# Kernel optimization log

Measured on AMD Instinct MI355X. Metric: run time of the kernel, lower is better.

Reference implementation:

```python
import jax, jax.numpy as jnp
import numpy as np

S, B, IN, H, OUT, L = 512, 64, 512, 1024, 512, 2


def setup_inputs() -> dict:
    key = jax.random.key(0)
    ks = jax.random.split(key, 16)
    s = lambda k, *shape: jax.random.normal(k, shape, dtype=jnp.float32) * 0.02
    inp = {
        "x": jax.random.normal(ks[0], (S, B, IN), dtype=jnp.float32),
        "h0": jnp.zeros((L, B, H), dtype=jnp.float32),
        # layer 0 (input -> hidden)
        "Ua0": s(ks[1], IN, H), "Uc0": s(ks[2], IN, H), "Uh0": s(ks[3], IN, H),
        "wa0": jax.random.normal(ks[4], (H,), dtype=jnp.float32) * 0.02,
        "wc0": jax.random.normal(ks[5], (H,), dtype=jnp.float32) * 0.02,
        "ba0": jnp.zeros((H,), jnp.float32), "bc0": jnp.zeros((H,), jnp.float32), "bh0": jnp.zeros((H,), jnp.float32),
        # layer 1 (hidden -> hidden)
        "Ua1": s(ks[6], H, H), "Uc1": s(ks[7], H, H), "Uh1": s(ks[8], H, H),
        "wa1": jax.random.normal(ks[9], (H,), dtype=jnp.float32) * 0.02,
        "wc1": jax.random.normal(ks[10], (H,), dtype=jnp.float32) * 0.02,
        "ba1": jnp.zeros((H,), jnp.float32), "bc1": jnp.zeros((H,), jnp.float32), "bh1": jnp.zeros((H,), jnp.float32),
        # decoder
        "Wdec": s(ks[11], H, OUT), "bdec": jnp.zeros((OUT,), jnp.float32),
    }
    return inp


def _brc_layer(x, h0, Ua, Uc, Uh, wa, wc, ba, bc, bh):
    """Bistable Recurrent Cell layer over time-major x: [S, B, in] -> ([S,B,H], [B,H])."""
    # Precompute all input-to-hidden projections as one big GEMM each.
    xa = x @ Ua + ba  # [S,B,H]
    xc = x @ Uc + bc
    xh = x @ Uh + bh

    def step(h, xs):
        xa_t, xc_t, xh_t = xs
        a = 1.0 + jnp.tanh(xa_t + wa * h)
        c = jax.nn.sigmoid(xc_t + wc * h)
        h_new = c * h + (1.0 - c) * jnp.tanh(xh_t + a * h)
        return h_new, h_new

    h_last, ys = jax.lax.scan(step, h0, (xa, xc, xh))
    return ys, h_last


def reference(x, h0, Ua0, Uc0, Uh0, wa0, wc0, ba0, bc0, bh0,
              Ua1, Uc1, Uh1, wa1, wc1, ba1, bc1, bh1, Wdec, bdec):
    y0, h0_last = _brc_layer(x, h0[0], Ua0, Uc0, Uh0, wa0, wc0, ba0, bc0, bh0)
    # dropout = 0.0 -> identity between layers
    y1, h1_last = _brc_layer(y0, h0[1], Ua1, Uc1, Uh1, wa1, wc1, ba1, bc1, bh1)
    out = y1 @ Wdec + bdec  # sequential_output=True -> decode every timestep
    hidden = jnp.stack([h0_last, h1_last])  # [L, B, H]
    return out, hidden
```

## Files before the change

kernel.cpp:

```cpp
#include <hip/hip_runtime.h>
#include <math.h>

#define S_DIM 512
#define B_DIM 64
#define IN_DIM 512
#define H_DIM 1024
#define OUT_DIM 512
#define BH (B_DIM * H_DIM)

typedef unsigned short ushort_t;
typedef unsigned int uint_t;
using f32x4 = __attribute__((ext_vector_type(4))) float;
using f16x8 = __attribute__((ext_vector_type(8))) _Float16;

#define LO_SCALE 2048.0f
#define LO_INV   (1.0f / 2048.0f)

__device__ __forceinline__ void split_f16(float v, ushort_t& hi, ushort_t& lo) {
    _Float16 h = (_Float16)v;
    float r = (v - (float)h) * LO_SCALE;
    _Float16 l = (_Float16)r;
    hi = __builtin_bit_cast(ushort_t, h);
    lo = __builtin_bit_cast(ushort_t, l);
}

__device__ __forceinline__ float frcp(float x) { return __builtin_amdgcn_rcpf(x); }
__device__ __forceinline__ float fsig(float z) { return frcp(1.f + __expf(-z)); }
__device__ __forceinline__ float ftanh(float z) { return 1.f - 2.f * frcp(1.f + __expf(2.f * z)); }

__device__ __forceinline__ void gload_lds16(const ushort_t* g, ushort_t* l) {
    __builtin_amdgcn_global_load_lds(
        (const __attribute__((address_space(1))) void*)g,
        (__attribute__((address_space(3))) void*)l, 16, 0, 0);
}

__global__ __launch_bounds__(256) void transpose_split_f16(
    const float* __restrict__ W, ushort_t* __restrict__ Whi, ushort_t* __restrict__ Wlo,
    int K, int N)
{
    __shared__ float tile[32][33];
    const int k0 = blockIdx.y * 32, n0 = blockIdx.x * 32;
    const int tx = threadIdx.x & 31, ty = threadIdx.x >> 5;
#pragma unroll
    for (int r = 0; r < 32; r += 8)
        tile[ty + r][tx] = W[(size_t)(k0 + ty + r) * N + n0 + tx];
    __syncthreads();
#pragma unroll
    for (int r = 0; r < 32; r += 8) {
        ushort_t hi, lo;
        split_f16(tile[tx][ty + r], hi, lo);
        const size_t o = (size_t)(n0 + ty + r) * K + k0 + tx;
        Whi[o] = hi;
        Wlo[o] = lo;
    }
}

__global__ __launch_bounds__(256) void convert_split_f16(
    const float* __restrict__ src, ushort_t* __restrict__ dhi, ushort_t* __restrict__ dlo,
    int n)
{
    const int i = (blockIdx.x * 256 + threadIdx.x) * 4;
    if (i < n) {
        float4 v = *(const float4*)(src + i);
        ushort4 h, l;
        split_f16(v.x, h.x, l.x); split_f16(v.y, h.y, l.y);
        split_f16(v.z, h.z, l.z); split_f16(v.w, h.w, l.w);
        *(ushort4*)(dhi + i) = h;
        *(ushort4*)(dlo + i) = l;
    }
}

__global__ __launch_bounds__(256, 2) void mfma_gemm3_split(
    const ushort_t* __restrict__ Ahi, const ushort_t* __restrict__ Alo,
    const ushort_t* __restrict__ Wh0, const ushort_t* __restrict__ Wl0,
    const ushort_t* __restrict__ Wh1, const ushort_t* __restrict__ Wl1,
    const ushort_t* __restrict__ Wh2, const ushort_t* __restrict__ Wl2,
    const float* __restrict__ b0, const float* __restrict__ b1, const float* __restrict__ b2,
    float* __restrict__ C0, float* __restrict__ C1, float* __restrict__ C2,
    int M, int N, int K)
{
    const int NB = N >> 7;
    const int inner = blockIdx.x % (3 * NB);
    const int mb = blockIdx.x / (3 * NB);
    const int nb = inner % NB;
    const int z  = inner / NB;

    const ushort_t* __restrict__ Wh = (z == 0) ? Wh0 : (z == 1) ? Wh1 : Wh2;
    const ushort_t* __restrict__ Wl = (z == 0) ? Wl0 : (z == 1) ? Wl1 : Wl2;
    const float* __restrict__ bias  = (z == 0) ? b0  : (z == 1) ? b1  : b2;
    float* __restrict__ C           = (z == 0) ? C0  : (z == 1) ? C1  : C2;

    __shared__ __align__(16) ushort_t AsH[2][128 * 32];
    __shared__ __align__(16) ushort_t AsL[2][128 * 32];
    __shared__ __align__(16) ushort_t BsH[2][128 * 32];
    __shared__ __align__(16) ushort_t BsL[2][128 * 32];

    const int tid  = threadIdx.x;
    const int lane = tid & 63;
    const int wave = tid >> 6;
    const int quad = lane >> 4;
    const int l16  = lane & 15;
    const int wm   = wave >> 1;
    const int wn   = wave & 1;

    const int row0 = mb * 128;
    const int col0 = nb * 128;

    f32x4 accP[4][4] = {};
    f32x4 accQ[4][4] = {};

    auto STAGE = [&](int buf, int k0) {
#pragma unroll
        for (int i = 0; i < 2; ++i) {
            const int c  = tid + i * 256;
            const int r  = c >> 2;
            const int kc = (c & 3) ^ ((r >> 1) & 3);
            const size_t ga = (size_t)(row0 + r) * K + k0 + kc * 8;
            const size_t gb = (size_t)(col0 + r) * K + k0 + kc * 8;
            gload_lds16(Ahi + ga, &AsH[buf][c * 8]);
            gload_lds16(Alo + ga, &AsL[buf][c * 8]);
            gload_lds16(Wh  + gb, &BsH[buf][c * 8]);
            gload_lds16(Wl  + gb, &BsL[buf][c * 8]);
        }
    };

    const int nt = K >> 5;
    STAGE(0, 0);
    int cur = 0;
    const int gq = (quad ^ ((l16 >> 1) & 3)) * 8;

    for (int t = 0; t < nt; ++t) {
        __syncthreads();
        if (t + 1 < nt) STAGE(cur ^ 1, (t + 1) << 5);

        f16x8 ah[4], al[4], bh[4], bl[4];
#pragma unroll
        for (int i = 0; i < 4; ++i) {
            const int ro = (wm * 64 + i * 16 + l16) * 32 + gq;
            ah[i] = *(const f16x8*)&AsH[cur][ro];
            al[i] = *(const f16x8*)&AsL[cur][ro];
        }
#pragma unroll
        for (int j = 0; j < 4; ++j) {
            const int ro = (wn * 64 + j * 16 + l16) * 32 + gq;
            bh[j] = *(const f16x8*)&BsH[cur][ro];
            bl[j] = *(const f16x8*)&BsL[cur][ro];
        }

#pragma unroll
        for (int i = 0; i < 4; ++i)
#pragma unroll
            for (int j = 0; j < 4; ++j) {
                accP[i][j] = __builtin_amdgcn_mfma_f32_16x16x32_f16(ah[i], bh[j], accP[i][j], 0, 0, 0);
                accQ[i][j] = __builtin_amdgcn_mfma_f32_16x16x32_f16(ah[i], bl[j], accQ[i][j], 0, 0, 0);
                accQ[i][j] = __builtin_amdgcn_mfma_f32_16x16x32_f16(al[i], bh[j], accQ[i][j], 0, 0, 0);
            }
        cur ^= 1;
    }

#pragma unroll
    for (int i = 0; i < 4; ++i) {
        const int row = row0 + wm * 64 + i * 16 + quad * 4;
#pragma unroll
        for (int j = 0; j < 4; ++j) {
            const int col = col0 + wn * 64 + j * 16 + l16;
            const float bv = bias[col];
#pragma unroll
            for (int r = 0; r < 4; ++r)
                C[(size_t)(row + r) * N + col] = accP[i][j][r] + accQ[i][j][r] * LO_INV + bv;
        }
    }
}

__global__ __launch_bounds__(256, 2) void mfma_gemm_dec(
    const ushort_t* __restrict__ A, const ushort_t* __restrict__ Wt,
    const float* __restrict__ bias, float* __restrict__ C,
    int M, int N, int K)
{
    const int NB = N >> 7;
    const int mb = blockIdx.x / NB;
    const int nb = blockIdx.x % NB;

    __shared__ __align__(16) ushort_t As[2][128 * 32];
    __shared__ __align__(16) ushort_t Bs[2][128 * 32];

    const int tid  = threadIdx.x;
    const int lane = tid & 63;
    const int wave = tid >> 6;
    const int quad = lane >> 4;
    const int l16  = lane & 15;
    const int wm   = wave >> 1;
    const int wn   = wave & 1;

    const int row0 = mb * 128;
    const int col0 = nb * 128;

    f32x4 acc[4][4] = {};

    auto STAGE = [&](int buf, int k0) {
#pragma unroll
        for (int i = 0; i < 2; ++i) {
            const int c  = tid + i * 256;
            const int r  = c >> 2;
            const int kc = (c & 3) ^ ((r >> 1) & 3);
            gload_lds16(A  + (size_t)(row0 + r) * K + k0 + kc * 8, &As[buf][c * 8]);
            gload_lds16(Wt + (size_t)(col0 + r) * K + k0 + kc * 8, &Bs[buf][c * 8]);
        }
    };

    const int nt = K >> 5;
    STAGE(0, 0);
    int cur = 0;
    const int gq = (quad ^ ((l16 >> 1) & 3)) * 8;

    for (int t = 0; t < nt; ++t) {
        __syncthreads();
        if (t + 1 < nt) STAGE(cur ^ 1, (t + 1) << 5);

        f16x8 af[4], bf[4];
#pragma unroll
        for (int i = 0; i < 4; ++i)
            af[i] = *(const f16x8*)&As[cur][(wm * 64 + i * 16 + l16) * 32 + gq];
#pragma unroll
        for (int j = 0; j < 4; ++j)
            bf[j] = *(const f16x8*)&Bs[cur][(wn * 64 + j * 16 + l16) * 32 + gq];

#pragma unroll
        for (int i = 0; i < 4; ++i)
#pragma unroll
            for (int j = 0; j < 4; ++j)
                acc[i][j] = __builtin_amdgcn_mfma_f32_16x16x32_f16(af[i], bf[j], acc[i][j], 0, 0, 0);
        cur ^= 1;
    }

#pragma unroll
    for (int i = 0; i < 4; ++i) {
        const int row = row0 + wm * 64 + i * 16 + quad * 4;
#pragma unroll
        for (int j = 0; j < 4; ++j) {
            const int col = col0 + wn * 64 + j * 16 + l16;
            const float bv = bias[col];
#pragma unroll
            for (int r = 0; r < 4; ++r)
                C[(size_t)(row + r) * N + col] = acc[i][j][r] + bv;
        }
    }
}

template <bool WRITE_LO>
__global__ __launch_bounds__(256) void brc_scan_v3(
    const float* __restrict__ xa, const float* __restrict__ xc,
    const float* __restrict__ xh, const float* __restrict__ wa,
    const float* __restrict__ wc, const float* __restrict__ h_in,
    ushort_t* __restrict__ yhi, ushort_t* __restrict__ ylo,
    float* __restrict__ h_out, int T_c)
{
    const int idx = blockIdx.x * 256 + threadIdx.x;
    const int j = idx & (H_DIM - 1);
    float h = h_in[idx];
    const float waj = wa[j], wcj = wc[j];

    float pa[8], pc[8], ph[8];
#pragma unroll
    for (int d = 0; d < 8; ++d) {
        const int dd = (d < T_c) ? d : 0;
        const size_t b = (size_t)dd * BH + idx;
        pa[d] = xa[b]; pc[d] = xc[b]; ph[d] = xh[b];
    }

#pragma unroll 8
    for (int t = 0; t < T_c; ++t) {
        const int s = t & 7;
        const float ca = pa[s], cc = pc[s], ch = ph[s];
        const int tn = t + 8;
        if (tn < T_c) {
            const size_t b = (size_t)tn * BH + idx;
            pa[s] = xa[b]; pc[s] = xc[b]; ph[s] = xh[b];
        }
        const float a = 1.f + ftanh(ca + waj * h);
        const float c = fsig(cc + wcj * h);
        h = c * h + (1.f - c) * ftanh(ch + a * h);

        ushort_t hh, hl;
        split_f16(h, hh, hl);
        const size_t ob = (size_t)t * BH + idx;
        yhi[ob] = hh;
        if (WRITE_LO) ylo[ob] = hl;
    }
    h_out[idx] = h;
}

extern "C" void kernel_launch(void* const* d_in, const int* in_sizes, int n_in,
                              void* d_out, int out_size, void* d_ws, size_t ws_size,
                              hipStream_t stream) {
    const float* x    = (const float*)d_in[0];
    const float* h0   = (const float*)d_in[1];
    const float* Ua0  = (const float*)d_in[2];
    const float* Uc0  = (const float*)d_in[3];
    const float* Uh0  = (const float*)d_in[4];
    const float* wa0  = (const float*)d_in[5];
    const float* wc0  = (const float*)d_in[6];
    const float* ba0  = (const float*)d_in[7];
    const float* bc0  = (const float*)d_in[8];
    const float* bh0  = (const float*)d_in[9];
    const float* Ua1  = (const float*)d_in[10];
    const float* Uc1  = (const float*)d_in[11];
    const float* Uh1  = (const float*)d_in[12];
    const float* wa1  = (const float*)d_in[13];
    const float* wc1  = (const float*)d_in[14];
    const float* ba1  = (const float*)d_in[15];
    const float* bc1  = (const float*)d_in[16];
    const float* bh1  = (const float*)d_in[17];
    const float* Wdec = (const float*)d_in[18];
    const float* bdec = (const float*)d_in[19];

    float* outF = (float*)d_out;
    float* out_seq  = outF;
    float* h_last0  = outF + (size_t)S_DIM * B_DIM * OUT_DIM;
    float* h_last1  = h_last0 + BH;

    char* wsb = (char*)d_ws;
    size_t off = 0;
    auto alloc = [&](size_t bytes) -> void* {
        void* p = wsb + off;
        off += (bytes + 255) & ~(size_t)255;
        return p;
    };
    const size_t szL0 = (size_t)IN_DIM * H_DIM;
    const size_t szL1 = (size_t)H_DIM * H_DIM;
    const size_t szD  = (size_t)H_DIM * OUT_DIM;
    ushort_t *Wa0h = (ushort_t*)alloc(szL0 * 2), *Wa0l = (ushort_t*)alloc(szL0 * 2);
    ushort_t *Wc0h = (ushort_t*)alloc(szL0 * 2), *Wc0l = (ushort_t*)alloc(szL0 * 2);
    ushort_t *Wh0h = (ushort_t*)alloc(szL0 * 2), *Wh0l = (ushort_t*)alloc(szL0 * 2);
    ushort_t *Wa1h = (ushort_t*)alloc(szL1 * 2), *Wa1l = (ushort_t*)alloc(szL1 * 2);
    ushort_t *Wc1h = (ushort_t*)alloc(szL1 * 2), *Wc1l = (ushort_t*)alloc(szL1 * 2);
    ushort_t *Wh1h = (ushort_t*)alloc(szL1 * 2), *Wh1l = (ushort_t*)alloc(szL1 * 2);
    ushort_t *Wdh  = (ushort_t*)alloc(szD * 2),  *Wdl  = (ushort_t*)alloc(szD * 2);

    const size_t perT = (size_t)2 * B_DIM * IN_DIM * 2 + (size_t)3 * BH * 4 + (size_t)3 * BH * 2;
    int T_c = 512;
    while (T_c > 1 && off + (size_t)T_c * perT + 4096 > ws_size) T_c >>= 1;
    const size_t chunk_elems = (size_t)T_c * BH;
    const size_t xchunk_elems = (size_t)T_c * B_DIM * IN_DIM;

    ushort_t* xhib = (ushort_t*)alloc(xchunk_elems * 2);
    ushort_t* xlob = (ushort_t*)alloc(xchunk_elems * 2);
    float* g_a = (float*)alloc(chunk_elems * 4);
    float* g_c = (float*)alloc(chunk_elems * 4);
    float* g_h = (float*)alloc(chunk_elems * 4);
    ushort_t* y0h = (ushort_t*)alloc(chunk_elems * 2);
    ushort_t* y0l = (ushort_t*)alloc(chunk_elems * 2);
    ushort_t* y1h = (ushort_t*)alloc(chunk_elems * 2);

    const int n_chunks = S_DIM / T_c;
    const int Mc = T_c * B_DIM;

    transpose_split_f16<<<dim3(H_DIM / 32, IN_DIM / 32), 256, 0, stream>>>(Ua0, Wa0h, Wa0l, IN_DIM, H_DIM);
    transpose_split_f16<<<dim3(H_DIM / 32, IN_DIM / 32), 256, 0, stream>>>(Uc0, Wc0h, Wc0l, IN_DIM, H_DIM);
    transpose_split_f16<<<dim3(H_DIM / 32, IN_DIM / 32), 256, 0, stream>>>(Uh0, Wh0h, Wh0l, IN_DIM, H_DIM);
    transpose_split_f16<<<dim3(H_DIM / 32, H_DIM / 32), 256, 0, stream>>>(Ua1, Wa1h, Wa1l, H_DIM, H_DIM);
    transpose_split_f16<<<dim3(H_DIM / 32, H_DIM / 32), 256, 0, stream>>>(Uc1, Wc1h, Wc1l, H_DIM, H_DIM);
    transpose_split_f16<<<dim3(H_DIM / 32, H_DIM / 32), 256, 0, stream>>>(Uh1, Wh1h, Wh1l, H_DIM, H_DIM);
    transpose_split_f16<<<dim3(OUT_DIM / 32, H_DIM / 32), 256, 0, stream>>>(Wdec, Wdh, Wdl, H_DIM, OUT_DIM);

    dim3 blk(256);
    const int grid_g = (H_DIM / 128) * (Mc / 128) * 3;
    const int grid_d = (OUT_DIM / 128) * (Mc / 128);
    dim3 grid_scan(BH / 256);

    for (int ci = 0; ci < n_chunks; ++ci) {
        const float* x_chunk = x + (size_t)ci * Mc * IN_DIM;
        float* out_chunk = out_seq + (size_t)ci * Mc * OUT_DIM;

        convert_split_f16<<<dim3((int)(xchunk_elems / 4 / 256)), blk, 0, stream>>>(
            x_chunk, xhib, xlob, (int)xchunk_elems);

        mfma_gemm3_split<<<dim3(grid_g), blk, 0, stream>>>(
            xhib, xlob, Wa0h, Wa0l, Wc0h, Wc0l, Wh0h, Wh0l,
            ba0, bc0, bh0, g_a, g_c, g_h, Mc, H_DIM, IN_DIM);
        brc_scan_v3<true><<<grid_scan, blk, 0, stream>>>(
            g_a, g_c, g_h, wa0, wc0, (ci == 0) ? h0 : h_last0, y0h, y0l, h_last0, T_c);

        mfma_gemm3_split<<<dim3(grid_g), blk, 0, stream>>>(
            y0h, y0l, Wa1h, Wa1l, Wc1h, Wc1l, Wh1h, Wh1l,
            ba1, bc1, bh1, g_a, g_c, g_h, Mc, H_DIM, H_DIM);
        brc_scan_v3<false><<<grid_scan, blk, 0, stream>>>(
            g_a, g_c, g_h, wa1, wc1, (ci == 0) ? (h0 + BH) : h_last1, y1h, nullptr, h_last1, T_c);

        mfma_gemm_dec<<<dim3(grid_d), blk, 0, stream>>>(
            y1h, Wdh, bdec, out_chunk, Mc, OUT_DIM, H_DIM);
    }
}
```

Baseline: 1.664 ms.

## Widen split-f16 GEMM tile to 128x256 with 512 threads and triple-buffered LDS

The three-way projection GEMM now uses 512-thread blocks, each computing a 128x256 tile with 8 waves, which halves the block count and doubles B-tile reuse. LDS staging moves from double to triple buffering with explicit vmcnt waits, so loads run two tiles ahead and only one barrier is needed per iteration. Address offsets are hoisted out of the loop, and setprio raises wave priority around the MFMA block. In exchange, shared memory rises to about 144KB, allowing one block per CU. With fewer blocks there is a risk of poorer wave occupancy and tail imbalance.

Measured after the change: 1.712 ms. +2.9%, slower.

```diff
diff --git a/kernel.cpp b/kernel.cpp
--- a/kernel.cpp
+++ b/kernel.cpp
@@ -70,7 +70,7 @@
     }
 }
 
-__global__ __launch_bounds__(256, 2) void mfma_gemm3_split(
+__global__ __launch_bounds__(512, 1) void mfma_gemm3_split(
     const ushort_t* __restrict__ Ahi, const ushort_t* __restrict__ Alo,
     const ushort_t* __restrict__ Wh0, const ushort_t* __restrict__ Wl0,
     const ushort_t* __restrict__ Wh1, const ushort_t* __restrict__ Wl1,
@@ -79,7 +79,7 @@
     float* __restrict__ C0, float* __restrict__ C1, float* __restrict__ C2,
     int M, int N, int K)
 {
-    const int NB = N >> 7;
+    const int NB = N >> 8;
     const int inner = blockIdx.x % (3 * NB);
     const int mb = blockIdx.x / (3 * NB);
     const int nb = inner % NB;
@@ -90,63 +90,83 @@
     const float* __restrict__ bias  = (z == 0) ? b0  : (z == 1) ? b1  : b2;
     float* __restrict__ C           = (z == 0) ? C0  : (z == 1) ? C1  : C2;
 
-    __shared__ __align__(16) ushort_t AsH[2][128 * 32];
-    __shared__ __align__(16) ushort_t AsL[2][128 * 32];
-    __shared__ __align__(16) ushort_t BsH[2][128 * 32];
-    __shared__ __align__(16) ushort_t BsL[2][128 * 32];
+    __shared__ __align__(16) ushort_t AsH[3][128 * 32];
+    __shared__ __align__(16) ushort_t AsL[3][128 * 32];
+    __shared__ __align__(16) ushort_t BsH[3][256 * 32];
+    __shared__ __align__(16) ushort_t BsL[3][256 * 32];
 
     const int tid  = threadIdx.x;
     const int lane = tid & 63;
     const int wave = tid >> 6;
     const int quad = lane >> 4;
     const int l16  = lane & 15;
-    const int wm   = wave >> 1;
-    const int wn   = wave & 1;
+    const int wm   = wave >> 2;
+    const int wn   = wave & 3;
 
     const int row0 = mb * 128;
-    const int col0 = nb * 128;
+    const int col0 = nb * 256;
 
     f32x4 accP[4][4] = {};
     f32x4 accQ[4][4] = {};
 
-    auto STAGE = [&](int buf, int k0) {
-#pragma unroll
-        for (int i = 0; i < 2; ++i) {
-            const int c  = tid + i * 256;
-            const int r  = c >> 2;
-            const int kc = (c & 3) ^ ((r >> 1) & 3);
-            const size_t ga = (size_t)(row0 + r) * K + k0 + kc * 8;
-            const size_t gb = (size_t)(col0 + r) * K + k0 + kc * 8;
-            gload_lds16(Ahi + ga, &AsH[buf][c * 8]);
-            gload_lds16(Alo + ga, &AsL[buf][c * 8]);
-            gload_lds16(Wh  + gb, &BsH[buf][c * 8]);
-            gload_lds16(Wl  + gb, &BsL[buf][c * 8]);
-        }
+    const int ca  = tid;
+    const int ra  = ca >> 2;
+    const int ka  = (ca & 3) ^ ((ra >> 1) & 3);
+    const size_t gaoff = (size_t)(row0 + ra) * K + ka * 8;
+
+    const int cb0 = tid,        rb0 = cb0 >> 2, kb0 = (cb0 & 3) ^ ((rb0 >> 1) & 3);
+    const int cb1 = tid + 512,  rb1 = cb1 >> 2, kb1 = (cb1 & 3) ^ ((rb1 >> 1) & 3);
+    const size_t gboff0 = (size_t)(col0 + rb0) * K + kb0 * 8;
+    const size_t gboff1 = (size_t)(col0 + rb1) * K + kb1 * 8;
+
+    auto STAGE = [&](int buf, int t) {
+        const int k0 = t << 5;
+        gload_lds16(Ahi + gaoff + k0, &AsH[buf][ca * 8]);
+        gload_lds16(Alo + gaoff + k0, &AsL[buf][ca * 8]);
+        gload_lds16(Wh + gboff0 + k0, &BsH[buf][cb0 * 8]);
+        gload_lds16(Wl + gboff0 + k0, &BsL[buf][cb0 * 8]);
+        gload_lds16(Wh + gboff1 + k0, &BsH[buf][cb1 * 8]);
+        gload_lds16(Wl + gboff1 + k0, &BsL[buf][cb1 * 8]);
     };
 
     const int nt = K >> 5;
     STAGE(0, 0);
+    STAGE(1, 1);
+
+    const int gq  = (quad ^ ((l16 >> 1) & 3)) * 8;
+    const int aro = (wm * 64 + l16) * 32 + gq;
+    const int bro = (wn * 64 + l16) * 32 + gq;
+
     int cur = 0;
-    const int gq = (quad ^ ((l16 >> 1) & 3)) * 8;
-
     for (int t = 0; t < nt; ++t) {
-        __syncthreads();
-        if (t + 1 < nt) STAGE(cur ^ 1, (t + 1) << 5);
+        if (t + 2 < nt) {
+            asm volatile("s_waitcnt vmcnt(6)" ::: "memory");
+        } else {
+            asm volatile("s_waitcnt vmcnt(0)" ::: "memory");
+        }
+        __builtin_amdgcn_sched_barrier(0);
+        __builtin_amdgcn_s_barrier();
+
+        if (t + 2 < nt) {
+            int nx = cur + 2; if (nx >= 3) nx -= 3;
+            STAGE(nx, t + 2);
+        }
 
         f16x8 ah[4], al[4], bh[4], bl[4];
 #pragma unroll
         for (int i = 0; i < 4; ++i) {
-            const int ro = (wm * 64 + i * 16 + l16) * 32 + gq;
+            const int ro = aro + i * 512;
             ah[i] = *(const f16x8*)&AsH[cur][ro];
             al[i] = *(const f16x8*)&AsL[cur][ro];
         }
 #pragma unroll
         for (int j = 0; j < 4; ++j) {
-            const int ro = (wn * 64 + j * 16 + l16) * 32 + gq;
+            const int ro = bro + j * 512;
             bh[j] = *(const f16x8*)&BsH[cur][ro];
             bl[j] = *(const f16x8*)&BsL[cur][ro];
         }
 
+        __builtin_amdgcn_s_setprio(1);
 #pragma unroll
         for (int i = 0; i < 4; ++i)
 #pragma unroll
@@ -155,7 +175,9 @@
                 accQ[i][j] = __builtin_amdgcn_mfma_f32_16x16x32_f16(ah[i], bl[j], accQ[i][j], 0, 0, 0);
                 accQ[i][j] = __builtin_amdgcn_mfma_f32_16x16x32_f16(al[i], bh[j], accQ[i][j], 0, 0, 0);
             }
-        cur ^= 1;
+        __builtin_amdgcn_s_setprio(0);
+
+        cur = (cur + 1 == 3) ? 0 : cur + 1;
     }
 
 #pragma unroll
@@ -363,8 +385,8 @@
     transpose_split_f16<<<dim3(H_DIM / 32, H_DIM / 32), 256, 0, stream>>>(Uh1, Wh1h, Wh1l, H_DIM, H_DIM);
     transpose_split_f16<<<dim3(OUT_DIM / 32, H_DIM / 32), 256, 0, stream>>>(Wdec, Wdh, Wdl, H_DIM, OUT_DIM);
 
-    dim3 blk(256);
-    const int grid_g = (H_DIM / 128) * (Mc / 128) * 3;
+    dim3 blk512(512), blk(256);
+    const int grid_g = (Mc / 128) * (H_DIM / 256) * 3;
     const int grid_d = (OUT_DIM / 128) * (Mc / 128);
     dim3 grid_scan(BH / 256);
 
@@ -375,13 +397,13 @@
         convert_split_f16<<<dim3((int)(xchunk_elems / 4 / 256)), blk, 0, stream>>>(
             x_chunk, xhib, xlob, (int)xchunk_elems);
 
-        mfma_gemm3_split<<<dim3(grid_g), blk, 0, stream>>>(
+        mfma_gemm3_split<<<dim3(grid_g), blk512, 0, stream>>>(
             xhib, xlob, Wa0h, Wa0l, Wc0h, Wc0l, Wh0h, Wh0l,
             ba0, bc0, bh0, g_a, g_c, g_h, Mc, H_DIM, IN_DIM);
         brc_scan_v3<true><<<grid_scan, blk, 0, stream>>>(
             g_a, g_c, g_h, wa0, wc0, (ci == 0) ? h0 : h_last0, y0h, y0l, h_last0, T_c);
 
-        mfma_gemm3_split<<<dim3(grid_g), blk, 0, stream>>>(
+        mfma_gemm3_split<<<dim3(grid_g), blk512, 0, stream>>>(
             y0h, y0l, Wa1h, Wa1l, Wc1h, Wc1l, Wh1h, Wh1l,
             ba1, bc1, bh1, g_a, g_c, g_h, Mc, H_DIM, H_DIM);
         brc_scan_v3<false><<<grid_scan, blk, 0, stream>>>(
```
